# Kernel tuning notes

Hardware: AMD Instinct MI355X
Metric: run time of the kernel (lower is better)

Reference implementation:

```python
import jax, jax.numpy as jnp
import numpy as np

B, T, D = 2, 2048, 1024
H, KVH = 16, 4
HD = D // H            # 64
E, TOPK, FFH = 8, 2, 2048
EPS = 1e-6
ROPE_THETA = 10000.0


def rmsnorm(x, w):
    return x * jax.lax.rsqrt(jnp.mean(x * x, axis=-1, keepdims=True) + EPS) * w


def rope(x, cos, sin):
    # x: (B, h, T, hd); pairs (even, odd) treated as complex, matching view_as_complex
    x2 = x.reshape(*x.shape[:-1], -1, 2)
    x0, x1 = x2[..., 0], x2[..., 1]
    o0 = x0 * cos - x1 * sin
    o1 = x0 * sin + x1 * cos
    return jnp.stack([o0, o1], axis=-1).reshape(x.shape)


def setup_inputs() -> dict:
    key = jax.random.key(0)
    ks = jax.random.split(key, 12)
    s = 0.02
    return {
        'x': jax.random.normal(ks[0], (B, T, D), dtype=jnp.float32),
        'attn_norm_w': jnp.ones((D,), jnp.float32),
        'wq': jax.random.normal(ks[1], (D, H * HD), jnp.float32) * s,
        'wk': jax.random.normal(ks[2], (D, KVH * HD), jnp.float32) * s,
        'wv': jax.random.normal(ks[3], (D, KVH * HD), jnp.float32) * s,
        'wo': jax.random.normal(ks[4], (D, D), jnp.float32) * s,
        'ffn_norm_w': jnp.ones((D,), jnp.float32),
        'gate_w': jax.random.normal(ks[5], (D, E), jnp.float32) * s,
        'gate_bias': jnp.zeros((E,), jnp.float32),  # e_score_correction_bias (aux-loss-free)
        'expert_w1': jax.random.normal(ks[6], (E, D, FFH), jnp.float32) * s,
        'expert_w2': jax.random.normal(ks[7], (E, FFH, D), jnp.float32) * s,
        'shared_w1': jax.random.normal(ks[8], (D, FFH), jnp.float32) * s,
        'shared_w2': jax.random.normal(ks[9], (FFH, D), jnp.float32) * s,
    }


def block_forward(x, attn_norm_w, wq, wk, wv, wo, ffn_norm_w, gate_w, gate_bias,
                  expert_w1, expert_w2, shared_w1, shared_w2):
    # ---- RoPE tables (precompute_freqs_cis, scaling_factor=1.0) ----
    half = HD // 2
    inv_freq = 1.0 / (ROPE_THETA ** (jnp.arange(half, dtype=jnp.float32) / half))
    t = jnp.arange(T, dtype=jnp.float32)
    fr = t[:, None] * inv_freq          # (T, half)
    cos, sin = jnp.cos(fr), jnp.sin(fr)

    # ---- attn_norm + GQA attention ----
    h = rmsnorm(x, attn_norm_w)
    q = (h @ wq).reshape(B, T, H, HD).transpose(0, 2, 1, 3)      # (B,H,T,HD)
    k = (h @ wk).reshape(B, T, KVH, HD).transpose(0, 2, 1, 3)    # (B,KVH,T,HD)
    v = (h @ wv).reshape(B, T, KVH, HD).transpose(0, 2, 1, 3)
    q = rope(q, cos, sin)
    k = rope(k, cos, sin)
    n_rep = H // KVH
    k = jnp.repeat(k, n_rep, axis=1)    # repeat_interleave over head dim
    v = jnp.repeat(v, n_rep, axis=1)
    att = jnp.einsum('bhqd,bhkd->bhqk', q, k) * (HD ** -0.5)
    causal = jnp.tril(jnp.ones((T, T), dtype=bool))
    att = jnp.where(causal, att, jnp.finfo(att.dtype).min)
    att = jax.nn.softmax(att, axis=-1)
    attn_out = jnp.einsum('bhqk,bhkd->bhqd', att, v).transpose(0, 2, 1, 3).reshape(B, T, D) @ wo
    x1 = x + attn_out

    # ---- ffn_norm + MoE feed-forward ----
    h2 = rmsnorm(x1, ffn_norm_w).reshape(-1, D)                  # (N, D)
    N = B * T
    shared = jax.nn.silu(h2 @ shared_w1) @ shared_w2             # 1 shared expert
    scores = jax.nn.sigmoid(h2 @ gate_w) + gate_bias             # sigmoid gate + correction bias
    topk_w, topk_i = jax.lax.top_k(scores, TOPK)
    topk_w = topk_w / (topk_w.sum(-1, keepdims=True) + 1e-20)    # norm_topk_prob; routed_scale=1.0
    combine = jnp.zeros((N, E), x.dtype).at[jnp.arange(N)[:, None], topk_i].add(topk_w)
    hmid = jax.nn.silu(jnp.einsum('nd,edh->enh', h2, expert_w1)) # (E,N,FFH)
    eout = jnp.einsum('enh,ehd->end', hmid, expert_w2)           # (E,N,D)
    routed = jnp.einsum('end,ne->nd', eout, combine)
    return x1 + (shared + routed).reshape(B, T, D)


def reference(x, attn_norm_w, wq, wk, wv, wo, ffn_norm_w, gate_w, gate_bias,
              expert_w1, expert_w2, shared_w1, shared_w2):
    return block_forward(x, attn_norm_w, wq, wk, wv, wo, ffn_norm_w, gate_w, gate_bias,
                         expert_w1, expert_w2, shared_w1, shared_w2)
```

## Files before the change

kernel.cpp:

```cpp
#include <hip/hip_runtime.h>
#include <math.h>

#define NTOK 4096
#define DM 1024
#define TSEQ 2048
#define NH 16
#define NKV 4
#define HDIM 64
#define NE 8
#define NFF 2048
#define QKVN 1536

typedef float f4v __attribute__((ext_vector_type(4)));
typedef short b8v __attribute__((ext_vector_type(8)));
typedef unsigned short u16;

__device__ __forceinline__ float silu_f(float v) { return v / (1.0f + expf(-v)); }

__device__ __forceinline__ u16 f2b(float f) {
    union { float f; unsigned u; } x{f};
    unsigned r = (x.u + 0x7FFFu + ((x.u >> 16) & 1u)) >> 16;
    return (u16)r;
}
__device__ __forceinline__ float b2f(u16 b) {
    union { unsigned u; float f; } x;
    x.u = ((unsigned)b) << 16;
    return x.f;
}

template <int MODE>
__global__ __launch_bounds__(256) void rmsnorm2_k(const float* __restrict__ x,
                                                  const float* __restrict__ w,
                                                  u16* __restrict__ oh, u16* __restrict__ ol,
                                                  float* __restrict__ of) {
    int row = blockIdx.x;
    int tid = threadIdx.x;
    const float4 v = ((const float4*)(x + (size_t)row * DM))[tid];
    float ss = v.x * v.x + v.y * v.y + v.z * v.z + v.w * v.w;
    for (int off = 32; off; off >>= 1) ss += __shfl_down(ss, off);
    __shared__ float red[4];
    if ((tid & 63) == 0) red[tid >> 6] = ss;
    __syncthreads();
    float tot = red[0] + red[1] + red[2] + red[3];
    float inv = rsqrtf(tot * (1.0f / DM) + 1e-6f);
    const float4 wv = ((const float4*)w)[tid];
    float o[4];
    o[0] = v.x * inv * wv.x; o[1] = v.y * inv * wv.y;
    o[2] = v.z * inv * wv.z; o[3] = v.w * inv * wv.w;
    if (MODE == 1) {
        float4 f; f.x = o[0]; f.y = o[1]; f.z = o[2]; f.w = o[3];
        ((float4*)(of + (size_t)row * DM))[tid] = f;
        ushort4 hb;
        hb.x = f2b(o[0]); hb.y = f2b(o[1]); hb.z = f2b(o[2]); hb.w = f2b(o[3]);
        ((ushort4*)(oh + (size_t)row * DM))[tid] = hb;
    } else {
        ushort4 hb, lb;
#pragma unroll
        for (int i = 0; i < 4; ++i) {
            u16 h = f2b(o[i]);
            u16 l = f2b(o[i] - b2f(h));
            ((u16*)&hb)[i] = h;
            ((u16*)&lb)[i] = l;
        }
        ((ushort4*)(oh + (size_t)row * DM))[tid] = hb;
        ((ushort4*)(ol + (size_t)row * DM))[tid] = lb;
    }
}

__global__ __launch_bounds__(256) void scast_k(const float* __restrict__ in, int stride,
                                               int colbase, int cols,
                                               u16* __restrict__ oh, u16* __restrict__ ol) {
    int idx = blockIdx.x * 256 + threadIdx.x;
    int cpr = cols >> 3;
    int row = idx / cpr;
    int cc = (idx - row * cpr) << 3;
    const float* p = in + (size_t)row * stride + colbase + cc;
    const float4 a = *(const float4*)p;
    const float4 b = *(const float4*)(p + 4);
    float vv[8] = {a.x, a.y, a.z, a.w, b.x, b.y, b.z, b.w};
    ushort4 h0, h1, l0, l1;
#pragma unroll
    for (int i = 0; i < 8; ++i) {
        u16 h = f2b(vv[i]);
        u16 l = f2b(vv[i] - b2f(h));
        if (i < 4) { ((u16*)&h0)[i] = h; ((u16*)&l0)[i] = l; }
        else       { ((u16*)&h1)[i - 4] = h; ((u16*)&l1)[i - 4] = l; }
    }
    u16* po = oh + (size_t)row * cols + cc;
    u16* pl = ol + (size_t)row * cols + cc;
    *(ushort4*)po = h0; *(ushort4*)(po + 4) = h1;
    *(ushort4*)pl = l0; *(ushort4*)(pl + 4) = l1;
}

__global__ __launch_bounds__(256) void vtrans_k(const float* __restrict__ qkv,
                                                u16* __restrict__ oh, u16* __restrict__ ol) {
    __shared__ float tl[32][33];
    int c0 = blockIdx.x << 5;
    int r0 = blockIdx.y << 5;
    int lr = threadIdx.x >> 3, lc = (threadIdx.x & 7) << 2;
    const float4 v = *(const float4*)&qkv[(size_t)(r0 + lr) * QKVN + 1280 + c0 + lc];
    tl[lr][lc] = v.x; tl[lr][lc + 1] = v.y; tl[lr][lc + 2] = v.z; tl[lr][lc + 3] = v.w;
    __syncthreads();
    int b = r0 >> 11;
    size_t obase = ((size_t)(b * 256 + c0 + lr)) * TSEQ + (r0 & 2047) + lc;
    ushort4 h4, l4;
#pragma unroll
    for (int i = 0; i < 4; ++i) {
        float f = tl[lc + i][lr];
        u16 h = f2b(f);
        u16 l = f2b(f - b2f(h));
        ((u16*)&h4)[i] = h; ((u16*)&l4)[i] = l;
    }
    *(ushort4*)&oh[obase] = h4;
    *(ushort4*)&ol[obase] = l4;
}

__global__ __launch_bounds__(256) void tcast2_k(const float* __restrict__ in,
                                                u16* __restrict__ oh, u16* __restrict__ ol,
                                                int R, int C) {
    __shared__ float tl[32][33];
    int r0 = blockIdx.y << 5, c0 = blockIdx.x << 5;
    int lr = threadIdx.x >> 3, lc = (threadIdx.x & 7) << 2;
    const float4 v = *(const float4*)&in[(size_t)(r0 + lr) * C + c0 + lc];
    tl[lr][lc] = v.x; tl[lr][lc + 1] = v.y; tl[lr][lc + 2] = v.z; tl[lr][lc + 3] = v.w;
    __syncthreads();
    ushort4 h4, l4;
#pragma unroll
    for (int i = 0; i < 4; ++i) {
        float f = tl[lc + i][lr];
        u16 h = f2b(f);
        u16 l = f2b(f - b2f(h));
        ((u16*)&h4)[i] = h; ((u16*)&l4)[i] = l;
    }
    size_t ob = (size_t)(c0 + lr) * R + r0 + lc;
    *(ushort4*)&oh[ob] = h4;
    *(ushort4*)&ol[ob] = l4;
}

__global__ __launch_bounds__(256) void tcast_k(const float* __restrict__ in,
                                               u16* __restrict__ out, int R, int C) {
    size_t boff = (size_t)blockIdx.z * R * C;
    in += boff; out += boff;
    __shared__ float tl[32][33];
    int r0 = blockIdx.y << 5, c0 = blockIdx.x << 5;
    int lr = threadIdx.x >> 3, lc = (threadIdx.x & 7) << 2;
    const float4 v = *(const float4*)&in[(size_t)(r0 + lr) * C + c0 + lc];
    tl[lr][lc] = v.x; tl[lr][lc + 1] = v.y; tl[lr][lc + 2] = v.z; tl[lr][lc + 3] = v.w;
    __syncthreads();
    ushort4 o;
    o.x = f2b(tl[lc + 0][lr]); o.y = f2b(tl[lc + 1][lr]);
    o.z = f2b(tl[lc + 2][lr]); o.w = f2b(tl[lc + 3][lr]);
    *(ushort4*)&out[(size_t)(c0 + lr) * R + r0 + lc] = o;
}

__global__ void rope2_k(float* __restrict__ x, int nheads, int colbase) {
    int idx = blockIdx.x * blockDim.x + threadIdx.x;
    int total = NTOK * nheads * 32;
    if (idx >= total) return;
    int j = idx & 31;
    int hh = (idx >> 5) % nheads;
    int n = idx / (nheads * 32);
    int t = n & (TSEQ - 1);
    float inv = expf(-(float)j * (0.03125f * logf(10000.0f)));
    float s, c;
    sincosf((float)t * inv, &s, &c);
    float* p = x + (size_t)n * QKVN + colbase + hh * 64 + j * 2;
    float x0 = p[0], x1 = p[1];
    p[0] = x0 * c - x1 * s;
    p[1] = x0 * s + x1 * c;
}

template <int EPI>
__global__ __launch_bounds__(256) void sgemm_k(const u16* __restrict__ Ah,
                                               const u16* __restrict__ Al,
                                               const u16* __restrict__ Bh,
                                               const u16* __restrict__ Bl,
                                               const float* __restrict__ Rr,
                                               float* __restrict__ C,
                                               int M, int N, int K) {
    __shared__ u16 Ash[128 * 40], Asl[128 * 40], Bsh[128 * 40], Bsl[128 * 40];
    int t = threadIdx.x;
    int l = t & 63, w = t >> 6;
    int wr = w >> 1, wc = w & 1;
    int n0 = blockIdx.x * 128, m0 = blockIdx.y * 128;
    int srow = t >> 2, scol = (t & 3) << 3;
    const u16 *agh[2], *agl[2], *bgh[2], *bgl[2];
#pragma unroll
    for (int i = 0; i < 2; ++i) {
        size_t ao = (size_t)(m0 + i * 64 + srow) * K + scol;
        size_t bo = (size_t)(n0 + i * 64 + srow) * K + scol;
        agh[i] = Ah + ao; agl[i] = Al + ao;
        bgh[i] = Bh + bo; bgl[i] = Bl + bo;
    }
    f4v acc[4][4];
#pragma unroll
    for (int m = 0; m < 4; ++m)
#pragma unroll
        for (int n = 0; n < 4; ++n) acc[m][n] = (f4v)0.0f;
    int kh_ = (l >> 4) << 3;
    for (int k0 = 0; k0 < K; k0 += 32) {
        b8v vah0 = *(const b8v*)(agh[0] + k0);
        b8v vah1 = *(const b8v*)(agh[1] + k0);
        b8v val0 = *(const b8v*)(agl[0] + k0);
        b8v val1 = *(const b8v*)(agl[1] + k0);
        b8v vbh0 = *(const b8v*)(bgh[0] + k0);
        b8v vbh1 = *(const b8v*)(bgh[1] + k0);
        b8v vbl0 = *(const b8v*)(bgl[0] + k0);
        b8v vbl1 = *(const b8v*)(bgl[1] + k0);
        __syncthreads();
        *(b8v*)&Ash[srow * 40 + scol] = vah0;
        *(b8v*)&Ash[(64 + srow) * 40 + scol] = vah1;
        *(b8v*)&Asl[srow * 40 + scol] = val0;
        *(b8v*)&Asl[(64 + srow) * 40 + scol] = val1;
        *(b8v*)&Bsh[srow * 40 + scol] = vbh0;
        *(b8v*)&Bsh[(64 + srow) * 40 + scol] = vbh1;
        *(b8v*)&Bsl[srow * 40 + scol] = vbl0;
        *(b8v*)&Bsl[(64 + srow) * 40 + scol] = vbl1;
        __syncthreads();
        b8v afh[4], afl[4], bfh[4], bfl[4];
#pragma unroll
        for (int m = 0; m < 4; ++m) {
            int ro = (wr * 64 + m * 16 + (l & 15)) * 40 + kh_;
            afh[m] = *(const b8v*)&Ash[ro];
            afl[m] = *(const b8v*)&Asl[ro];
        }
#pragma unroll
        for (int n = 0; n < 4; ++n) {
            int ro = (wc * 64 + n * 16 + (l & 15)) * 40 + kh_;
            bfh[n] = *(const b8v*)&Bsh[ro];
            bfl[n] = *(const b8v*)&Bsl[ro];
        }
#pragma unroll
        for (int m = 0; m < 4; ++m)
#pragma unroll
            for (int n = 0; n < 4; ++n) {
                acc[m][n] = __builtin_amdgcn_mfma_f32_16x16x32_bf16(afl[m], bfh[n], acc[m][n], 0, 0, 0);
                acc[m][n] = __builtin_amdgcn_mfma_f32_16x16x32_bf16(afh[m], bfl[n], acc[m][n], 0, 0, 0);
                acc[m][n] = __builtin_amdgcn_mfma_f32_16x16x32_bf16(afh[m], bfh[n], acc[m][n], 0, 0, 0);
            }
    }
#pragma unroll
    for (int m = 0; m < 4; ++m) {
        int r0l = m0 + wr * 64 + m * 16 + ((l >> 4) << 2);
#pragma unroll
        for (int n = 0; n < 4; ++n) {
            int col = n0 + wc * 64 + n * 16 + (l & 15);
            f4v c = acc[m][n];
#pragma unroll
            for (int j = 0; j < 4; ++j) {
                size_t idx = (size_t)(r0l + j) * N + col;
                float v = c[j];
                if (EPI == 2) v += Rr[idx];
                C[idx] = v;
            }
        }
    }
}

__global__ __launch_bounds__(256) void mattn_k(const u16* __restrict__ qh, const u16* __restrict__ ql,
                                               const u16* __restrict__ kh, const u16* __restrict__ kl,
                                               const u16* __restrict__ vth, const u16* __restrict__ vtl,
                                               float* __restrict__ o) {
    __shared__ short plds[4][2][16][72];
    int t = threadIdx.x, l = t & 63, w = t >> 6;
    int bh = blockIdx.y, b = bh >> 4, h = bh & 15, kvh = h >> 2;
    size_t bT = (size_t)b * TSEQ;
    int lx = l & 15, lg = l >> 4;
#pragma unroll
    for (int half = 0; half < 2; ++half) {
        int qt = half ? (31 - blockIdx.x) : blockIdx.x;
        int q0 = qt * 64;
        b8v qfh[2], qfl[2];
        {
            size_t qo = (bT + q0 + w * 16 + lx) * DM + h * 64 + lg * 8;
            qfh[0] = *(const b8v*)(qh + qo);
            qfh[1] = *(const b8v*)(qh + qo + 32);
            qfl[0] = *(const b8v*)(ql + qo);
            qfl[1] = *(const b8v*)(ql + qo + 32);
        }
        f4v acc[4];
#pragma unroll
        for (int ht = 0; ht < 4; ++ht) acc[ht] = (f4v)0.0f;
        float l_r[4] = {0.0f, 0.0f, 0.0f, 0.0f};
        int qg[4];
#pragma unroll
        for (int r = 0; r < 4; ++r) qg[r] = q0 + w * 16 + lg * 4 + r;
        int ntile = qt + 1;
        for (int kt = 0; kt < ntile; ++kt) {
            int kv0 = kt << 6;
            f4v s[4];
#pragma unroll
            for (int st = 0; st < 4; ++st) {
                size_t ko = (bT + kv0 + st * 16 + lx) * 256 + kvh * 64 + lg * 8;
                b8v kf0h = *(const b8v*)(kh + ko);
                b8v kf1h = *(const b8v*)(kh + ko + 32);
                b8v kf0l = *(const b8v*)(kl + ko);
                b8v kf1l = *(const b8v*)(kl + ko + 32);
                f4v ss = (f4v)0.0f;
                ss = __builtin_amdgcn_mfma_f32_16x16x32_bf16(qfl[0], kf0h, ss, 0, 0, 0);
                ss = __builtin_amdgcn_mfma_f32_16x16x32_bf16(qfh[0], kf0l, ss, 0, 0, 0);
                ss = __builtin_amdgcn_mfma_f32_16x16x32_bf16(qfh[0], kf0h, ss, 0, 0, 0);
                ss = __builtin_amdgcn_mfma_f32_16x16x32_bf16(qfl[1], kf1h, ss, 0, 0, 0);
                ss = __builtin_amdgcn_mfma_f32_16x16x32_bf16(qfh[1], kf1l, ss, 0, 0, 0);
                ss = __builtin_amdgcn_mfma_f32_16x16x32_bf16(qfh[1], kf1h, ss, 0, 0, 0);
                s[st] = ss;
            }
            b8v vh0[4], vh1[4], vl0[4], vl1[4];
#pragma unroll
            for (int ht = 0; ht < 4; ++ht) {
                size_t vo = ((size_t)(b * 4 + kvh) * 64 + ht * 16 + lx) * TSEQ + kv0 + lg * 8;
                vh0[ht] = *(const b8v*)(vth + vo);
                vh1[ht] = *(const b8v*)(vth + vo + 32);
                vl0[ht] = *(const b8v*)(vtl + vo);
                vl1[ht] = *(const b8v*)(vtl + vo + 32);
            }
#pragma unroll
            for (int st = 0; st < 4; ++st)
#pragma unroll
                for (int r = 0; r < 4; ++r) {
                    float v = s[st][r] * 0.125f;
                    float p = (kv0 + st * 16 + lx > qg[r])
                                  ? 0.0f
                                  : __expf(fminf(v, 60.0f));
                    l_r[r] += p;
                    u16 ph = f2b(p);
                    u16 pl = f2b(p - b2f(ph));
                    plds[w][0][lg * 4 + r][st * 16 + lx] = (short)ph;
                    plds[w][1][lg * 4 + r][st * 16 + lx] = (short)pl;
                }
            __threadfence_block();
            __builtin_amdgcn_sched_barrier(0);
            b8v pf0h = *(const b8v*)&plds[w][0][lx][lg * 8];
            b8v pf1h = *(const b8v*)&plds[w][0][lx][32 + lg * 8];
            b8v pf0l = *(const b8v*)&plds[w][1][lx][lg * 8];
            b8v pf1l = *(const b8v*)&plds[w][1][lx][32 + lg * 8];
            __builtin_amdgcn_sched_barrier(0);
#pragma unroll
            for (int ht = 0; ht < 4; ++ht) {
                acc[ht] = __builtin_amdgcn_mfma_f32_16x16x32_bf16(pf0l, vh0[ht], acc[ht], 0, 0, 0);
                acc[ht] = __builtin_amdgcn_mfma_f32_16x16x32_bf16(pf0h, vl0[ht], acc[ht], 0, 0, 0);
                acc[ht] = __builtin_amdgcn_mfma_f32_16x16x32_bf16(pf0h, vh0[ht], acc[ht], 0, 0, 0);
                acc[ht] = __builtin_amdgcn_mfma_f32_16x16x32_bf16(pf1l, vh1[ht], acc[ht], 0, 0, 0);
                acc[ht] = __builtin_amdgcn_mfma_f32_16x16x32_bf16(pf1h, vl1[ht], acc[ht], 0, 0, 0);
                acc[ht] = __builtin_amdgcn_mfma_f32_16x16x32_bf16(pf1h, vh1[ht], acc[ht], 0, 0, 0);
            }
        }
#pragma unroll
        for (int r = 0; r < 4; ++r) {
            float rs = l_r[r];
            rs += __shfl_xor(rs, 1);
            rs += __shfl_xor(rs, 2);
            rs += __shfl_xor(rs, 4);
            rs += __shfl_xor(rs, 8);
            float rinv = 1.0f / rs;
#pragma unroll
            for (int ht = 0; ht < 4; ++ht) {
                o[(bT + q0 + w * 16 + lg * 4 + r) * DM + h * 64 + ht * 16 + lx] =
                    acc[ht][r] * rinv;
            }
        }
    }
}

__global__ __launch_bounds__(64) void gate_k(const float* __restrict__ h2,
                                             const float* __restrict__ gw,
                                             const float* __restrict__ gb,
                                             int* __restrict__ top2i,
                                             float* __restrict__ top2w,
                                             int* __restrict__ counts) {
    int n = blockIdx.x;
    int lane = threadIdx.x;
    float acc[8] = {};
    for (int d = lane; d < DM; d += 64) {
        float hv = h2[(size_t)n * DM + d];
        const float4 g0 = ((const float4*)&gw[d * 8])[0];
        const float4 g1 = ((const float4*)&gw[d * 8])[1];
        acc[0] = fmaf(hv, g0.x, acc[0]); acc[1] = fmaf(hv, g0.y, acc[1]);
        acc[2] = fmaf(hv, g0.z, acc[2]); acc[3] = fmaf(hv, g0.w, acc[3]);
        acc[4] = fmaf(hv, g1.x, acc[4]); acc[5] = fmaf(hv, g1.y, acc[5]);
        acc[6] = fmaf(hv, g1.z, acc[6]); acc[7] = fmaf(hv, g1.w, acc[7]);
    }
#pragma unroll
    for (int e = 0; e < 8; ++e)
        for (int off = 32; off; off >>= 1) acc[e] += __shfl_down(acc[e], off);
    if (lane == 0) {
        float s[8];
#pragma unroll
        for (int e = 0; e < 8; ++e) s[e] = 1.0f / (1.0f + expf(-acc[e])) + gb[e];
        int i0 = 0;
#pragma unroll
        for (int e = 1; e < 8; ++e) if (s[e] > s[i0]) i0 = e;
        int i1 = (i0 == 0) ? 1 : 0;
#pragma unroll
        for (int e = 0; e < 8; ++e) if (e != i0 && s[e] > s[i1]) i1 = e;
        float w0 = s[i0], w1 = s[i1];
        float norm = 1.0f / (w0 + w1 + 1e-20f);
        top2i[n * 2] = i0; top2i[n * 2 + 1] = i1;
        top2w[n * 2] = w0 * norm; top2w[n * 2 + 1] = w1 * norm;
        atomicAdd(&counts[i0], 1);
        atomicAdd(&counts[i1], 1);
    }
}

__global__ void zero16_k(int* p) { if (threadIdx.x < 16) p[threadIdx.x] = 0; }

__global__ void scan_k(const int* __restrict__ counts, int* __restrict__ segs) {
    if (threadIdx.x == 0) {
        segs[0] = 0;
        for (int e = 0; e < NE; ++e) segs[e + 1] = segs[e] + counts[e];
    }
}

__global__ void scatter_k(const int* __restrict__ top2i, const float* __restrict__ top2w,
                          const int* __restrict__ segs, int* __restrict__ cursor,
                          int* __restrict__ list, float* __restrict__ wslot,
                          int* __restrict__ slot_of) {
    int idx = blockIdx.x * blockDim.x + threadIdx.x;
    if (idx >= NTOK * 2) return;
    int e = top2i[idx];
    int pos = segs[e] + atomicAdd(&cursor[e], 1);
    list[pos] = idx >> 1;
    wslot[pos] = top2w[idx];
    slot_of[idx] = pos;
}

template <int EPI, int MOE, int GATHER>
__global__ __launch_bounds__(256) void mgemm_k(const u16* __restrict__ A,
                                               const u16* __restrict__ Bt,
                                               const float* __restrict__ R,
                                               const float* __restrict__ wslot,
                                               const int* __restrict__ list,
                                               const int* __restrict__ segs,
                                               float* __restrict__ Cf,
                                               u16* __restrict__ Cb,
                                               int M, int N, int K) {
    __shared__ u16 As[128 * 40];
    __shared__ u16 Bs[128 * 40];
    int e = MOE ? blockIdx.z : 0;
    int base = 0, cnt = M;
    if (MOE) { base = segs[e]; cnt = segs[e + 1] - base; }
    int m0 = blockIdx.y * 128;
    if (m0 >= cnt) return;
    int n0 = blockIdx.x * 128;
    const u16* Bte = Bt + (size_t)e * N * K;
    int t = threadIdx.x;
    int l = t & 63, w = t >> 6;
    int wr = w >> 1, wc = w & 1;
    int srow = t >> 2, scol = (t & 3) << 3;
    const u16* ag[2];
    const u16* bg[2];
#pragma unroll
    for (int i = 0; i < 2; ++i) {
        int r = m0 + i * 64 + srow;
        int ar;
        if (MOE) {
            int rc = r < cnt ? r : cnt - 1;
            ar = GATHER ? list[base + rc] : base + rc;
        } else {
            ar = r;
        }
        ag[i] = A + (size_t)ar * K + scol;
        bg[i] = Bte + (size_t)(n0 + i * 64 + srow) * K + scol;
    }
    f4v acc[4][4];
#pragma unroll
    for (int m = 0; m < 4; ++m)
#pragma unroll
        for (int n = 0; n < 4; ++n) acc[m][n] = (f4v)0.0f;
    int kh = (l >> 4) << 3;
    for (int k0 = 0; k0 < K; k0 += 32) {
        b8v va0 = *(const b8v*)(ag[0] + k0);
        b8v va1 = *(const b8v*)(ag[1] + k0);
        b8v vb0 = *(const b8v*)(bg[0] + k0);
        b8v vb1 = *(const b8v*)(bg[1] + k0);
        __syncthreads();
        *(b8v*)&As[srow * 40 + scol] = va0;
        *(b8v*)&As[(64 + srow) * 40 + scol] = va1;
        *(b8v*)&Bs[srow * 40 + scol] = vb0;
        *(b8v*)&Bs[(64 + srow) * 40 + scol] = vb1;
        __syncthreads();
        b8v af[4], bf[4];
#pragma unroll
        for (int m = 0; m < 4; ++m)
            af[m] = *(const b8v*)&As[(wr * 64 + m * 16 + (l & 15)) * 40 + kh];
#pragma unroll
        for (int n = 0; n < 4; ++n)
            bf[n] = *(const b8v*)&Bs[(wc * 64 + n * 16 + (l & 15)) * 40 + kh];
#pragma unroll
        for (int m = 0; m < 4; ++m)
#pragma unroll
            for (int n = 0; n < 4; ++n)
                acc[m][n] = __builtin_amdgcn_mfma_f32_16x16x32_bf16(af[m], bf[n], acc[m][n], 0, 0, 0);
    }
#pragma unroll
    for (int m = 0; m < 4; ++m) {
        int r0l = m0 + wr * 64 + m * 16 + ((l >> 4) << 2);
#pragma unroll
        for (int n = 0; n < 4; ++n) {
            int col = n0 + wc * 64 + n * 16 + (l & 15);
            f4v c = acc[m][n];
#pragma unroll
            for (int j = 0; j < 4; ++j) {
                int row = r0l + j;
                if (MOE && row >= cnt) continue;
                float v = c[j];
                if (EPI == 1) {
                    v = silu_f(v);
                    Cb[(size_t)(base + row) * N + col] = f2b(v);
                } else if (EPI == 2) {
                    size_t idx = (size_t)row * N + col;
                    Cf[idx] = v + R[idx];
                } else if (EPI == 3) {
                    Cf[(size_t)(base + row) * N + col] = v * wslot[base + row];
                } else {
                    Cf[(size_t)row * N + col] = v;
                }
            }
        }
    }
}

__global__ __launch_bounds__(256) void combine_k(const float* __restrict__ eout,
                                                 const int* __restrict__ slot_of,
                                                 float* __restrict__ out) {
    int idx = blockIdx.x * blockDim.x + threadIdx.x;
    int n = idx >> 8;
    int c = idx & 255;
    const float4 a = ((const float4*)(eout + (size_t)slot_of[n * 2] * DM))[c];
    const float4 b = ((const float4*)(eout + (size_t)slot_of[n * 2 + 1] * DM))[c];
    float4 o = ((float4*)out)[idx];
    o.x += a.x + b.x; o.y += a.y + b.y; o.z += a.z + b.z; o.w += a.w + b.w;
    ((float4*)out)[idx] = o;
}

extern "C" void kernel_launch(void* const* d_in, const int* in_sizes, int n_in,
                              void* d_out, int out_size, void* d_ws, size_t ws_size,
                              hipStream_t stream) {
    (void)in_sizes; (void)n_in; (void)out_size; (void)ws_size;
    const float* x   = (const float*)d_in[0];
    const float* anw = (const float*)d_in[1];
    const float* wq  = (const float*)d_in[2];
    const float* wk  = (const float*)d_in[3];
    const float* wv  = (const float*)d_in[4];
    const float* wo  = (const float*)d_in[5];
    const float* fnw = (const float*)d_in[6];
    const float* gw  = (const float*)d_in[7];
    const float* gb  = (const float*)d_in[8];
    const float* ew1 = (const float*)d_in[9];
    const float* ew2 = (const float*)d_in[10];
    const float* sw1 = (const float*)d_in[11];
    const float* sw2 = (const float*)d_in[12];
    float* out = (float*)d_out;

#define WSOFF(mb) ((char*)d_ws + (size_t)(mb) * 1048576)
    u16* qkvT_h = (u16*)WSOFF(0);
    u16* qkvT_l = (u16*)WSOFF(3);
    u16* woT_h  = (u16*)WSOFF(6);
    u16* woT_l  = (u16*)WSOFF(8);
    u16* sw1t   = (u16*)WSOFF(10);
    u16* sw2t   = (u16*)WSOFF(14);
    u16* ew1t   = (u16*)WSOFF(18);
    u16* ew2t   = (u16*)WSOFF(50);
    float* qkv  = (float*)WSOFF(82);
    float* ao   = (float*)WSOFF(82);
    float* h2f  = (float*)WSOFF(82);
    u16* h_hi   = (u16*)WSOFF(106);
    u16* h_lo   = (u16*)WSOFF(114);
    u16* ao_hi  = (u16*)WSOFF(106);
    u16* ao_lo  = (u16*)WSOFF(114);
    u16* q_hi   = (u16*)WSOFF(122);
    u16* q_lo   = (u16*)WSOFF(130);
    u16* k_hi   = (u16*)WSOFF(138);
    u16* k_lo   = (u16*)WSOFF(140);
    u16* vT_hi  = (u16*)WSOFF(142);
    u16* vT_lo  = (u16*)WSOFF(144);
    float* x1   = (float*)WSOFF(146);
    u16* h2b    = (u16*)WSOFF(162);
    u16* midb   = (u16*)WSOFF(170);
    u16* hmidb  = (u16*)WSOFF(122);
    float* eoutb = (float*)WSOFF(154);
    int* meta0  = (int*)WSOFF(186);
    int*   top2i  = meta0;
    float* top2w  = (float*)(meta0 + 8192);
    int*   counts = meta0 + 16384;
    int*   cursor = meta0 + 16392;
    int*   segs   = meta0 + 16400;
    int*   list   = meta0 + 16416;
    float* wslot  = (float*)(meta0 + 16416 + 8192);
    int*   slot_of = meta0 + 16416 + 16384;

    tcast2_k<<<dim3(32, 32), 256, 0, stream>>>(wq, qkvT_h, qkvT_l, DM, 1024);
    tcast2_k<<<dim3(8, 32), 256, 0, stream>>>(wk, qkvT_h + 1024 * 1024, qkvT_l + 1024 * 1024, DM, 256);
    tcast2_k<<<dim3(8, 32), 256, 0, stream>>>(wv, qkvT_h + 1280 * 1024, qkvT_l + 1280 * 1024, DM, 256);
    tcast2_k<<<dim3(32, 32), 256, 0, stream>>>(wo, woT_h, woT_l, DM, DM);
    tcast_k<<<dim3(NFF / 32, DM / 32, 1), 256, 0, stream>>>(sw1, sw1t, DM, NFF);
    tcast_k<<<dim3(DM / 32, NFF / 32, 1), 256, 0, stream>>>(sw2, sw2t, NFF, DM);
    tcast_k<<<dim3(NFF / 32, DM / 32, NE), 256, 0, stream>>>(ew1, ew1t, DM, NFF);
    tcast_k<<<dim3(DM / 32, NFF / 32, NE), 256, 0, stream>>>(ew2, ew2t, NFF, DM);

    rmsnorm2_k<0><<<NTOK, 256, 0, stream>>>(x, anw, h_hi, h_lo, nullptr);
    sgemm_k<0><<<dim3(QKVN / 128, NTOK / 128), 256, 0, stream>>>(
        h_hi, h_lo, qkvT_h, qkvT_l, nullptr, qkv, NTOK, QKVN, DM);
    rope2_k<<<(NTOK * NH * 32 + 255) / 256, 256, 0, stream>>>(qkv, NH, 0);
    rope2_k<<<(NTOK * NKV * 32 + 255) / 256, 256, 0, stream>>>(qkv, NKV, 1024);
    scast_k<<<2048, 256, 0, stream>>>(qkv, QKVN, 0, 1024, q_hi, q_lo);
    scast_k<<<512, 256, 0, stream>>>(qkv, QKVN, 1024, 256, k_hi, k_lo);
    vtrans_k<<<dim3(8, 128), 256, 0, stream>>>(qkv, vT_hi, vT_lo);
    mattn_k<<<dim3(TSEQ / 128, 32), 256, 0, stream>>>(q_hi, q_lo, k_hi, k_lo, vT_hi, vT_lo, ao);
    scast_k<<<2048, 256, 0, stream>>>(ao, DM, 0, DM, ao_hi, ao_lo);
    sgemm_k<2><<<dim3(DM / 128, NTOK / 128), 256, 0, stream>>>(
        ao_hi, ao_lo, woT_h, woT_l, x, x1, NTOK, DM, DM);
    rmsnorm2_k<1><<<NTOK, 256, 0, stream>>>(x1, fnw, h2b, nullptr, h2f);
    zero16_k<<<1, 64, 0, stream>>>(counts);
    gate_k<<<NTOK, 64, 0, stream>>>(h2f, gw, gb, top2i, top2w, counts);
    scan_k<<<1, 1, 0, stream>>>(counts, segs);
    scatter_k<<<32, 256, 0, stream>>>(top2i, top2w, segs, cursor, list, wslot, slot_of);
    mgemm_k<1, 0, 0><<<dim3(NFF / 128, NTOK / 128, 1), 256, 0, stream>>>(
        h2b, sw1t, nullptr, nullptr, nullptr, nullptr, nullptr, midb, NTOK, NFF, DM);
    mgemm_k<2, 0, 0><<<dim3(DM / 128, NTOK / 128, 1), 256, 0, stream>>>(
        midb, sw2t, x1, nullptr, nullptr, nullptr, out, nullptr, NTOK, DM, NFF);
    mgemm_k<1, 1, 1><<<dim3(NFF / 128, NTOK / 128, NE), 256, 0, stream>>>(
        h2b, ew1t, nullptr, nullptr, list, segs, nullptr, hmidb, NTOK, NFF, DM);
    mgemm_k<3, 1, 0><<<dim3(DM / 128, NTOK / 128, NE), 256, 0, stream>>>(
        hmidb, ew2t, nullptr, wslot, nullptr, segs, eoutb, nullptr, 2 * NTOK, DM, NFF);
    combine_k<<<NTOK, 256, 0, stream>>>(eoutb, slot_of, out);
#undef WSOFF
}
```

Baseline: 1.029 ms.

## Fuse RoPE into split-cast, async LDS loads with XOR swizzle, attention emits bf16 pairs

RoPE is now applied inside the hi/lo split kernel using a precomputed cos/sin table, which replaces two in-place RoPE passes and two cast passes. The GEMM kernels load tiles with global_load_lds straight into an XOR-swizzled, unpadded LDS layout, dropping the register staging. The attention kernel launches one q-tile per block instead of pairing tiles for balance, and writes bf16 hi/lo outputs directly, which removes the separate cast pass. The P matrix split now truncates instead of rounding, which may cost a little accuracy.

Measured after the change: 1.230 ms. +19.5%, slower.

```diff
diff --git a/kernel.cpp b/kernel.cpp
--- a/kernel.cpp
+++ b/kernel.cpp
@@ -22,10 +22,20 @@
     unsigned r = (x.u + 0x7FFFu + ((x.u >> 16) & 1u)) >> 16;
     return (u16)r;
 }
+__device__ __forceinline__ u16 f2bt(float f) {
+    union { float f; unsigned u; } x{f};
+    return (u16)(x.u >> 16);
+}
 __device__ __forceinline__ float b2f(u16 b) {
     union { unsigned u; float f; } x;
     x.u = ((unsigned)b) << 16;
     return x.f;
+}
+
+__device__ __forceinline__ void gload16(const void* g, void* l) {
+    typedef __attribute__((address_space(1))) const void gv;
+    typedef __attribute__((address_space(3))) void lv;
+    __builtin_amdgcn_global_load_lds((gv*)g, (lv*)l, 16, 0, 0);
 }
 
 template <int MODE>
@@ -67,22 +77,44 @@
     }
 }
 
-__global__ __launch_bounds__(256) void scast_k(const float* __restrict__ in, int stride,
-                                               int colbase, int cols,
-                                               u16* __restrict__ oh, u16* __restrict__ ol) {
+__global__ __launch_bounds__(256) void ropetab_k(float* __restrict__ tab) {
+    int idx = blockIdx.x * 256 + threadIdx.x;
+    if (idx >= TSEQ * 32) return;
+    int t = idx >> 5, j = idx & 31;
+    float inv = expf(-(float)j * (0.03125f * logf(10000.0f)));
+    float s, c;
+    sincosf((float)t * inv, &s, &c);
+    tab[t * 64 + j * 2] = c;
+    tab[t * 64 + j * 2 + 1] = s;
+}
+
+__global__ __launch_bounds__(256) void rope_split_k(const float* __restrict__ qkv,
+                                                    const float* __restrict__ tab,
+                                                    int colbase, int cols,
+                                                    u16* __restrict__ oh, u16* __restrict__ ol) {
     int idx = blockIdx.x * 256 + threadIdx.x;
     int cpr = cols >> 3;
     int row = idx / cpr;
     int cc = (idx - row * cpr) << 3;
-    const float* p = in + (size_t)row * stride + colbase + cc;
+    const float* p = qkv + (size_t)row * QKVN + colbase + cc;
     const float4 a = *(const float4*)p;
     const float4 b = *(const float4*)(p + 4);
     float vv[8] = {a.x, a.y, a.z, a.w, b.x, b.y, b.z, b.w};
+    int tpos = row & (TSEQ - 1);
+    const float* tb = tab + tpos * 64 + ((cc & 63) >> 1) * 2;
+    float ov[8];
+#pragma unroll
+    for (int q = 0; q < 4; ++q) {
+        float c = tb[q * 2], s = tb[q * 2 + 1];
+        float x0 = vv[2 * q], x1 = vv[2 * q + 1];
+        ov[2 * q] = x0 * c - x1 * s;
+        ov[2 * q + 1] = x0 * s + x1 * c;
+    }
     ushort4 h0, h1, l0, l1;
 #pragma unroll
     for (int i = 0; i < 8; ++i) {
-        u16 h = f2b(vv[i]);
-        u16 l = f2b(vv[i] - b2f(h));
+        u16 h = f2b(ov[i]);
+        u16 l = f2b(ov[i] - b2f(h));
         if (i < 4) { ((u16*)&h0)[i] = h; ((u16*)&l0)[i] = l; }
         else       { ((u16*)&h1)[i - 4] = h; ((u16*)&l1)[i - 4] = l; }
     }
@@ -153,23 +185,6 @@
     *(ushort4*)&out[(size_t)(c0 + lr) * R + r0 + lc] = o;
 }
 
-__global__ void rope2_k(float* __restrict__ x, int nheads, int colbase) {
-    int idx = blockIdx.x * blockDim.x + threadIdx.x;
-    int total = NTOK * nheads * 32;
-    if (idx >= total) return;
-    int j = idx & 31;
-    int hh = (idx >> 5) % nheads;
-    int n = idx / (nheads * 32);
-    int t = n & (TSEQ - 1);
-    float inv = expf(-(float)j * (0.03125f * logf(10000.0f)));
-    float s, c;
-    sincosf((float)t * inv, &s, &c);
-    float* p = x + (size_t)n * QKVN + colbase + hh * 64 + j * 2;
-    float x0 = p[0], x1 = p[1];
-    p[0] = x0 * c - x1 * s;
-    p[1] = x0 * s + x1 * c;
-}
-
 template <int EPI>
 __global__ __launch_bounds__(256) void sgemm_k(const u16* __restrict__ Ah,
                                                const u16* __restrict__ Al,
@@ -178,17 +193,19 @@
                                                const float* __restrict__ Rr,
                                                float* __restrict__ C,
                                                int M, int N, int K) {
-    __shared__ u16 Ash[128 * 40], Asl[128 * 40], Bsh[128 * 40], Bsl[128 * 40];
+    __shared__ u16 Ash[128 * 32], Asl[128 * 32], Bsh[128 * 32], Bsl[128 * 32];
     int t = threadIdx.x;
     int l = t & 63, w = t >> 6;
     int wr = w >> 1, wc = w & 1;
+    int lx = l & 15, lg = l >> 4;
     int n0 = blockIdx.x * 128, m0 = blockIdx.y * 128;
-    int srow = t >> 2, scol = (t & 3) << 3;
+    int srow = t >> 2;
+    int cs = (t & 3) ^ ((srow & 3) ^ ((t >> 4) & 3));
     const u16 *agh[2], *agl[2], *bgh[2], *bgl[2];
 #pragma unroll
     for (int i = 0; i < 2; ++i) {
-        size_t ao = (size_t)(m0 + i * 64 + srow) * K + scol;
-        size_t bo = (size_t)(n0 + i * 64 + srow) * K + scol;
+        size_t ao = (size_t)(m0 + i * 64 + srow) * K + cs * 8;
+        size_t bo = (size_t)(n0 + i * 64 + srow) * K + cs * 8;
         agh[i] = Ah + ao; agl[i] = Al + ao;
         bgh[i] = Bh + bo; bgl[i] = Bl + bo;
     }
@@ -197,38 +214,35 @@
     for (int m = 0; m < 4; ++m)
 #pragma unroll
         for (int n = 0; n < 4; ++n) acc[m][n] = (f4v)0.0f;
-    int kh_ = (l >> 4) << 3;
+    int keyr = (lx & 3) ^ ((lx >> 2) & 3);
+    int chb = (lg ^ keyr) << 4;
+    int aoff[4], boff[4];
+#pragma unroll
+    for (int m = 0; m < 4; ++m) aoff[m] = ((wr * 64 + m * 16 + lx) << 6) + chb;
+#pragma unroll
+    for (int n = 0; n < 4; ++n) boff[n] = ((wc * 64 + n * 16 + lx) << 6) + chb;
+    int wb = w * 1024;
     for (int k0 = 0; k0 < K; k0 += 32) {
-        b8v vah0 = *(const b8v*)(agh[0] + k0);
-        b8v vah1 = *(const b8v*)(agh[1] + k0);
-        b8v val0 = *(const b8v*)(agl[0] + k0);
-        b8v val1 = *(const b8v*)(agl[1] + k0);
-        b8v vbh0 = *(const b8v*)(bgh[0] + k0);
-        b8v vbh1 = *(const b8v*)(bgh[1] + k0);
-        b8v vbl0 = *(const b8v*)(bgl[0] + k0);
-        b8v vbl1 = *(const b8v*)(bgl[1] + k0);
         __syncthreads();
-        *(b8v*)&Ash[srow * 40 + scol] = vah0;
-        *(b8v*)&Ash[(64 + srow) * 40 + scol] = vah1;
-        *(b8v*)&Asl[srow * 40 + scol] = val0;
-        *(b8v*)&Asl[(64 + srow) * 40 + scol] = val1;
-        *(b8v*)&Bsh[srow * 40 + scol] = vbh0;
-        *(b8v*)&Bsh[(64 + srow) * 40 + scol] = vbh1;
-        *(b8v*)&Bsl[srow * 40 + scol] = vbl0;
-        *(b8v*)&Bsl[(64 + srow) * 40 + scol] = vbl1;
+        gload16(agh[0] + k0, (char*)Ash + wb);
+        gload16(agh[1] + k0, (char*)Ash + wb + 4096);
+        gload16(agl[0] + k0, (char*)Asl + wb);
+        gload16(agl[1] + k0, (char*)Asl + wb + 4096);
+        gload16(bgh[0] + k0, (char*)Bsh + wb);
+        gload16(bgh[1] + k0, (char*)Bsh + wb + 4096);
+        gload16(bgl[0] + k0, (char*)Bsl + wb);
+        gload16(bgl[1] + k0, (char*)Bsl + wb + 4096);
         __syncthreads();
         b8v afh[4], afl[4], bfh[4], bfl[4];
 #pragma unroll
         for (int m = 0; m < 4; ++m) {
-            int ro = (wr * 64 + m * 16 + (l & 15)) * 40 + kh_;
-            afh[m] = *(const b8v*)&Ash[ro];
-            afl[m] = *(const b8v*)&Asl[ro];
+            afh[m] = *(const b8v*)((const char*)Ash + aoff[m]);
+            afl[m] = *(const b8v*)((const char*)Asl + aoff[m]);
         }
 #pragma unroll
         for (int n = 0; n < 4; ++n) {
-            int ro = (wc * 64 + n * 16 + (l & 15)) * 40 + kh_;
-            bfh[n] = *(const b8v*)&Bsh[ro];
-            bfl[n] = *(const b8v*)&Bsl[ro];
+            bfh[n] = *(const b8v*)((const char*)Bsh + boff[n]);
+            bfl[n] = *(const b8v*)((const char*)Bsl + boff[n]);
         }
 #pragma unroll
         for (int m = 0; m < 4; ++m)
@@ -260,104 +274,102 @@
 __global__ __launch_bounds__(256) void mattn_k(const u16* __restrict__ qh, const u16* __restrict__ ql,
                                                const u16* __restrict__ kh, const u16* __restrict__ kl,
                                                const u16* __restrict__ vth, const u16* __restrict__ vtl,
-                                               float* __restrict__ o) {
+                                               u16* __restrict__ aoh, u16* __restrict__ aol) {
     __shared__ short plds[4][2][16][72];
     int t = threadIdx.x, l = t & 63, w = t >> 6;
     int bh = blockIdx.y, b = bh >> 4, h = bh & 15, kvh = h >> 2;
     size_t bT = (size_t)b * TSEQ;
     int lx = l & 15, lg = l >> 4;
-#pragma unroll
-    for (int half = 0; half < 2; ++half) {
-        int qt = half ? (31 - blockIdx.x) : blockIdx.x;
-        int q0 = qt * 64;
-        b8v qfh[2], qfl[2];
-        {
-            size_t qo = (bT + q0 + w * 16 + lx) * DM + h * 64 + lg * 8;
-            qfh[0] = *(const b8v*)(qh + qo);
-            qfh[1] = *(const b8v*)(qh + qo + 32);
-            qfl[0] = *(const b8v*)(ql + qo);
-            qfl[1] = *(const b8v*)(ql + qo + 32);
-        }
-        f4v acc[4];
-#pragma unroll
-        for (int ht = 0; ht < 4; ++ht) acc[ht] = (f4v)0.0f;
-        float l_r[4] = {0.0f, 0.0f, 0.0f, 0.0f};
-        int qg[4];
-#pragma unroll
-        for (int r = 0; r < 4; ++r) qg[r] = q0 + w * 16 + lg * 4 + r;
-        int ntile = qt + 1;
-        for (int kt = 0; kt < ntile; ++kt) {
-            int kv0 = kt << 6;
-            f4v s[4];
-#pragma unroll
-            for (int st = 0; st < 4; ++st) {
-                size_t ko = (bT + kv0 + st * 16 + lx) * 256 + kvh * 64 + lg * 8;
-                b8v kf0h = *(const b8v*)(kh + ko);
-                b8v kf1h = *(const b8v*)(kh + ko + 32);
-                b8v kf0l = *(const b8v*)(kl + ko);
-                b8v kf1l = *(const b8v*)(kl + ko + 32);
-                f4v ss = (f4v)0.0f;
-                ss = __builtin_amdgcn_mfma_f32_16x16x32_bf16(qfl[0], kf0h, ss, 0, 0, 0);
-                ss = __builtin_amdgcn_mfma_f32_16x16x32_bf16(qfh[0], kf0l, ss, 0, 0, 0);
-                ss = __builtin_amdgcn_mfma_f32_16x16x32_bf16(qfh[0], kf0h, ss, 0, 0, 0);
-                ss = __builtin_amdgcn_mfma_f32_16x16x32_bf16(qfl[1], kf1h, ss, 0, 0, 0);
-                ss = __builtin_amdgcn_mfma_f32_16x16x32_bf16(qfh[1], kf1l, ss, 0, 0, 0);
-                ss = __builtin_amdgcn_mfma_f32_16x16x32_bf16(qfh[1], kf1h, ss, 0, 0, 0);
-                s[st] = ss;
+    int qt = 31 - blockIdx.x;
+    int q0 = qt * 64;
+    b8v qfh[2], qfl[2];
+    {
+        size_t qo = (bT + q0 + w * 16 + lx) * DM + h * 64 + lg * 8;
+        qfh[0] = *(const b8v*)(qh + qo);
+        qfh[1] = *(const b8v*)(qh + qo + 32);
+        qfl[0] = *(const b8v*)(ql + qo);
+        qfl[1] = *(const b8v*)(ql + qo + 32);
+    }
+    f4v acc[4];
+#pragma unroll
+    for (int ht = 0; ht < 4; ++ht) acc[ht] = (f4v)0.0f;
+    float l_r[4] = {0.0f, 0.0f, 0.0f, 0.0f};
+    int qg[4];
+#pragma unroll
+    for (int r = 0; r < 4; ++r) qg[r] = q0 + w * 16 + lg * 4 + r;
+    int ntile = qt + 1;
+    for (int kt = 0; kt < ntile; ++kt) {
+        int kv0 = kt << 6;
+        f4v s[4];
+#pragma unroll
+        for (int st = 0; st < 4; ++st) {
+            size_t ko = (bT + kv0 + st * 16 + lx) * 256 + kvh * 64 + lg * 8;
+            b8v kf0h = *(const b8v*)(kh + ko);
+            b8v kf1h = *(const b8v*)(kh + ko + 32);
+            b8v kf0l = *(const b8v*)(kl + ko);
+            b8v kf1l = *(const b8v*)(kl + ko + 32);
+            f4v ss = (f4v)0.0f;
+            ss = __builtin_amdgcn_mfma_f32_16x16x32_bf16(qfl[0], kf0h, ss, 0, 0, 0);
+            ss = __builtin_amdgcn_mfma_f32_16x16x32_bf16(qfh[0], kf0l, ss, 0, 0, 0);
+            ss = __builtin_amdgcn_mfma_f32_16x16x32_bf16(qfh[0], kf0h, ss, 0, 0, 0);
+            ss = __builtin_amdgcn_mfma_f32_16x16x32_bf16(qfl[1], kf1h, ss, 0, 0, 0);
+            ss = __builtin_amdgcn_mfma_f32_16x16x32_bf16(qfh[1], kf1l, ss, 0, 0, 0);
+            ss = __builtin_amdgcn_mfma_f32_16x16x32_bf16(qfh[1], kf1h, ss, 0, 0, 0);
+            s[st] = ss;
+        }
+        b8v vh0[4], vh1[4], vl0[4], vl1[4];
+#pragma unroll
+        for (int ht = 0; ht < 4; ++ht) {
+            size_t vo = ((size_t)(b * 4 + kvh) * 64 + ht * 16 + lx) * TSEQ + kv0 + lg * 8;
+            vh0[ht] = *(const b8v*)(vth + vo);
+            vh1[ht] = *(const b8v*)(vth + vo + 32);
+            vl0[ht] = *(const b8v*)(vtl + vo);
+            vl1[ht] = *(const b8v*)(vtl + vo + 32);
+        }
+#pragma unroll
+        for (int st = 0; st < 4; ++st)
+#pragma unroll
+            for (int r = 0; r < 4; ++r) {
+                float v = s[st][r] * 0.125f;
+                float p = (kv0 + st * 16 + lx > qg[r]) ? 0.0f : __expf(fminf(v, 60.0f));
+                l_r[r] += p;
+                u16 ph = f2bt(p);
+                u16 pl = f2bt(p - b2f(ph));
+                plds[w][0][lg * 4 + r][st * 16 + lx] = (short)ph;
+                plds[w][1][lg * 4 + r][st * 16 + lx] = (short)pl;
             }
-            b8v vh0[4], vh1[4], vl0[4], vl1[4];
-#pragma unroll
-            for (int ht = 0; ht < 4; ++ht) {
-                size_t vo = ((size_t)(b * 4 + kvh) * 64 + ht * 16 + lx) * TSEQ + kv0 + lg * 8;
-                vh0[ht] = *(const b8v*)(vth + vo);
-                vh1[ht] = *(const b8v*)(vth + vo + 32);
-                vl0[ht] = *(const b8v*)(vtl + vo);
-                vl1[ht] = *(const b8v*)(vtl + vo + 32);
-            }
-#pragma unroll
-            for (int st = 0; st < 4; ++st)
-#pragma unroll
-                for (int r = 0; r < 4; ++r) {
-                    float v = s[st][r] * 0.125f;
-                    float p = (kv0 + st * 16 + lx > qg[r])
-                                  ? 0.0f
-                                  : __expf(fminf(v, 60.0f));
-                    l_r[r] += p;
-                    u16 ph = f2b(p);
-                    u16 pl = f2b(p - b2f(ph));
-                    plds[w][0][lg * 4 + r][st * 16 + lx] = (short)ph;
-                    plds[w][1][lg * 4 + r][st * 16 + lx] = (short)pl;
-                }
-            __threadfence_block();
-            __builtin_amdgcn_sched_barrier(0);
-            b8v pf0h = *(const b8v*)&plds[w][0][lx][lg * 8];
-            b8v pf1h = *(const b8v*)&plds[w][0][lx][32 + lg * 8];
-            b8v pf0l = *(const b8v*)&plds[w][1][lx][lg * 8];
-            b8v pf1l = *(const b8v*)&plds[w][1][lx][32 + lg * 8];
-            __builtin_amdgcn_sched_barrier(0);
-#pragma unroll
-            for (int ht = 0; ht < 4; ++ht) {
-                acc[ht] = __builtin_amdgcn_mfma_f32_16x16x32_bf16(pf0l, vh0[ht], acc[ht], 0, 0, 0);
-                acc[ht] = __builtin_amdgcn_mfma_f32_16x16x32_bf16(pf0h, vl0[ht], acc[ht], 0, 0, 0);
-                acc[ht] = __builtin_amdgcn_mfma_f32_16x16x32_bf16(pf0h, vh0[ht], acc[ht], 0, 0, 0);
-                acc[ht] = __builtin_amdgcn_mfma_f32_16x16x32_bf16(pf1l, vh1[ht], acc[ht], 0, 0, 0);
-                acc[ht] = __builtin_amdgcn_mfma_f32_16x16x32_bf16(pf1h, vl1[ht], acc[ht], 0, 0, 0);
-                acc[ht] = __builtin_amdgcn_mfma_f32_16x16x32_bf16(pf1h, vh1[ht], acc[ht], 0, 0, 0);
-            }
-        }
-#pragma unroll
-        for (int r = 0; r < 4; ++r) {
-            float rs = l_r[r];
-            rs += __shfl_xor(rs, 1);
-            rs += __shfl_xor(rs, 2);
-            rs += __shfl_xor(rs, 4);
-            rs += __shfl_xor(rs, 8);
-            float rinv = 1.0f / rs;
-#pragma unroll
-            for (int ht = 0; ht < 4; ++ht) {
-                o[(bT + q0 + w * 16 + lg * 4 + r) * DM + h * 64 + ht * 16 + lx] =
-                    acc[ht][r] * rinv;
-            }
+        __threadfence_block();
+        __builtin_amdgcn_sched_barrier(0);
+        b8v pf0h = *(const b8v*)&plds[w][0][lx][lg * 8];
+        b8v pf1h = *(const b8v*)&plds[w][0][lx][32 + lg * 8];
+        b8v pf0l = *(const b8v*)&plds[w][1][lx][lg * 8];
+        b8v pf1l = *(const b8v*)&plds[w][1][lx][32 + lg * 8];
+        __builtin_amdgcn_sched_barrier(0);
+#pragma unroll
+        for (int ht = 0; ht < 4; ++ht) {
+            acc[ht] = __builtin_amdgcn_mfma_f32_16x16x32_bf16(pf0l, vh0[ht], acc[ht], 0, 0, 0);
+            acc[ht] = __builtin_amdgcn_mfma_f32_16x16x32_bf16(pf0h, vl0[ht], acc[ht], 0, 0, 0);
+            acc[ht] = __builtin_amdgcn_mfma_f32_16x16x32_bf16(pf0h, vh0[ht], acc[ht], 0, 0, 0);
+            acc[ht] = __builtin_amdgcn_mfma_f32_16x16x32_bf16(pf1l, vh1[ht], acc[ht], 0, 0, 0);
+            acc[ht] = __builtin_amdgcn_mfma_f32_16x16x32_bf16(pf1h, vl1[ht], acc[ht], 0, 0, 0);
+            acc[ht] = __builtin_amdgcn_mfma_f32_16x16x32_bf16(pf1h, vh1[ht], acc[ht], 0, 0, 0);
+        }
+    }
+#pragma unroll
+    for (int r = 0; r < 4; ++r) {
+        float rs = l_r[r];
+        rs += __shfl_xor(rs, 1);
+        rs += __shfl_xor(rs, 2);
+        rs += __shfl_xor(rs, 4);
+        rs += __shfl_xor(rs, 8);
+        float rinv = 1.0f / rs;
+#pragma unroll
+        for (int ht = 0; ht < 4; ++ht) {
+            size_t idx = (bT + q0 + w * 16 + lg * 4 + r) * DM + h * 64 + ht * 16 + lx;
+            float v = acc[ht][r] * rinv;
+            u16 hh = f2b(v);
+            aoh[idx] = hh;
+            aol[idx] = f2b(v - b2f(hh));
         }
     }
 }
@@ -434,8 +446,8 @@
                                                float* __restrict__ Cf,
                                                u16* __restrict__ Cb,
                                                int M, int N, int K) {
-    __shared__ u16 As[128 * 40];
-    __shared__ u16 Bs[128 * 40];
+    __shared__ u16 As[128 * 32];
+    __shared__ u16 Bs[128 * 32];
     int e = MOE ? blockIdx.z : 0;
     int base = 0, cnt = M;
     if (MOE) { base = segs[e]; cnt = segs[e + 1] - base; }
@@ -446,7 +458,9 @@
     int t = threadIdx.x;
     int l = t & 63, w = t >> 6;
     int wr = w >> 1, wc = w & 1;
-    int srow = t >> 2, scol = (t & 3) << 3;
+    int lx = l & 15, lg = l >> 4;
+    int srow = t >> 2;
+    int cs = (t & 3) ^ ((srow & 3) ^ ((t >> 4) & 3));
     const u16* ag[2];
     const u16* bg[2];
 #pragma unroll
@@ -459,33 +473,34 @@
         } else {
             ar = r;
         }
-        ag[i] = A + (size_t)ar * K + scol;
-        bg[i] = Bte + (size_t)(n0 + i * 64 + srow) * K + scol;
+        ag[i] = A + (size_t)ar * K + cs * 8;
+        bg[i] = Bte + (size_t)(n0 + i * 64 + srow) * K + cs * 8;
     }
     f4v acc[4][4];
 #pragma unroll
     for (int m = 0; m < 4; ++m)
 #pragma unroll
         for (int n = 0; n < 4; ++n) acc[m][n] = (f4v)0.0f;
-    int kh = (l >> 4) << 3;
+    int keyr = (lx & 3) ^ ((lx >> 2) & 3);
+    int chb = (lg ^ keyr) << 4;
+    int aoff[4], boff[4];
+#pragma unroll
+    for (int m = 0; m < 4; ++m) aoff[m] = ((wr * 64 + m * 16 + lx) << 6) + chb;
+#pragma unroll
+    for (int n = 0; n < 4; ++n) boff[n] = ((wc * 64 + n * 16 + lx) << 6) + chb;
+    int wb = w * 1024;
     for (int k0 = 0; k0 < K; k0 += 32) {
-        b8v va0 = *(const b8v*)(ag[0] + k0);
-        b8v va1 = *(const b8v*)(ag[1] + k0);
-        b8v vb0 = *(const b8v*)(bg[0] + k0);
-        b8v vb1 = *(const b8v*)(bg[1] + k0);
         __syncthreads();
-        *(b8v*)&As[srow * 40 + scol] = va0;
-        *(b8v*)&As[(64 + srow) * 40 + scol] = va1;
-        *(b8v*)&Bs[srow * 40 + scol] = vb0;
-        *(b8v*)&Bs[(64 + srow) * 40 + scol] = vb1;
+        gload16(ag[0] + k0, (char*)As + wb);
+        gload16(ag[1] + k0, (char*)As + wb + 4096);
+        gload16(bg[0] + k0, (char*)Bs + wb);
+        gload16(bg[1] + k0, (char*)Bs + wb + 4096);
         __syncthreads();
         b8v af[4], bf[4];
 #pragma unroll
-        for (int m = 0; m < 4; ++m)
-            af[m] = *(const b8v*)&As[(wr * 64 + m * 16 + (l & 15)) * 40 + kh];
-#pragma unroll
-        for (int n = 0; n < 4; ++n)
-            bf[n] = *(const b8v*)&Bs[(wc * 64 + n * 16 + (l & 15)) * 40 + kh];
+        for (int m = 0; m < 4; ++m) af[m] = *(const b8v*)((const char*)As + aoff[m]);
+#pragma unroll
+        for (int n = 0; n < 4; ++n) bf[n] = *(const b8v*)((const char*)Bs + boff[n]);
 #pragma unroll
         for (int m = 0; m < 4; ++m)
 #pragma unroll
@@ -562,7 +577,6 @@
     u16* ew1t   = (u16*)WSOFF(18);
     u16* ew2t   = (u16*)WSOFF(50);
     float* qkv  = (float*)WSOFF(82);
-    float* ao   = (float*)WSOFF(82);
     float* h2f  = (float*)WSOFF(82);
     u16* h_hi   = (u16*)WSOFF(106);
     u16* h_lo   = (u16*)WSOFF(114);
@@ -588,7 +602,9 @@
     int*   list   = meta0 + 16416;
     float* wslot  = (float*)(meta0 + 16416 + 8192);
     int*   slot_of = meta0 + 16416 + 16384;
-
+    float* ropetab = (float*)WSOFF(190);
+
+    ropetab_k<<<256, 256, 0, stream>>>(ropetab);
     tcast2_k<<<dim3(32, 32), 256, 0, stream>>>(wq, qkvT_h, qkvT_l, DM, 1024);
     tcast2_k<<<dim3(8, 32), 256, 0, stream>>>(wk, qkvT_h + 1024 * 1024, qkvT_l + 1024 * 1024, DM, 256);
     tcast2_k<<<dim3(8, 32), 256, 0, stream>>>(wv, qkvT_h + 1280 * 1024, qkvT_l + 1280 * 1024, DM, 256);
@@ -601,13 +617,10 @@
     rmsnorm2_k<0><<<NTOK, 256, 0, stream>>>(x, anw, h_hi, h_lo, nullptr);
     sgemm_k<0><<<dim3(QKVN / 128, NTOK / 128), 256, 0, stream>>>(
         h_hi, h_lo, qkvT_h, qkvT_l, nullptr, qkv, NTOK, QKVN, DM);
-    rope2_k<<<(NTOK * NH * 32 + 255) / 256, 256, 0, stream>>>(qkv, NH, 0);
-    rope2_k<<<(NTOK * NKV * 32 + 255) / 256, 256, 0, stream>>>(qkv, NKV, 1024);
-    scast_k<<<2048, 256, 0, stream>>>(qkv, QKVN, 0, 1024, q_hi, q_lo);
-    scast_k<<<512, 256, 0, stream>>>(qkv, QKVN, 1024, 256, k_hi, k_lo);
+    rope_split_k<<<2048, 256, 0, stream>>>(qkv, ropetab, 0, 1024, q_hi, q_lo);
+    rope_split_k<<<512, 256, 0, stream>>>(qkv, ropetab, 1024, 256, k_hi, k_lo);
     vtrans_k<<<dim3(8, 128), 256, 0, stream>>>(qkv, vT_hi, vT_lo);
-    mattn_k<<<dim3(TSEQ / 128, 32), 256, 0, stream>>>(q_hi, q_lo, k_hi, k_lo, vT_hi, vT_lo, ao);
-    scast_k<<<2048, 256, 0, stream>>>(ao, DM, 0, DM, ao_hi, ao_lo);
+    mattn_k<<<dim3(32, 32), 256, 0, stream>>>(q_hi, q_lo, k_hi, k_lo, vT_hi, vT_lo, ao_hi, ao_lo);
     sgemm_k<2><<<dim3(DM / 128, NTOK / 128), 256, 0, stream>>>(
         ao_hi, ao_lo, woT_h, woT_l, x, x1, NTOK, DM, DM);
     rmsnorm2_k<1><<<NTOK, 256, 0, stream>>>(x1, fnw, h2b, nullptr, h2f);
```
